# Performance work log

Measured on AMD Instinct MI355X. Metric: run time of the kernel, lower is better.

The kernel has to match this reference:

```python
import jax, jax.numpy as jnp
import numpy as np

EPS = 1e-12  # F.normalize default eps

def _l2norm(x, axis):
    n = jnp.maximum(jnp.linalg.norm(x, axis=axis, keepdims=True), EPS)
    return x / n

def setup_inputs() -> dict:
    key = jax.random.key(0)
    k1, k2 = jax.random.split(key)
    B, G, D, K = 256, 100, 768, 128
    h = jax.random.normal(k1, (B, G, D), dtype=jnp.float32)
    duplicate_pooling = jax.random.normal(k2, (G, D, K), dtype=jnp.float32)
    out_extrap = jnp.zeros((B, G, K), dtype=jnp.float32)
    return {"h": h, "duplicate_pooling": duplicate_pooling, "out_extrap": out_extrap}

def reference(h, duplicate_pooling, out_extrap):
    # normalize=True: L2-normalize each h[:, i, :] over feature dim (dim=1 of the
    # flattened [B, D] view == last axis), and each w_i = W[i] over dim=0 (the D axis).
    hn = _l2norm(h, axis=-1)                       # [B, G, D]
    wn = _l2norm(duplicate_pooling, axis=1)        # [G, D, K]
    # Fused grouped batched GEMM over all G groups at once.
    out = jnp.einsum('bgd,gdk->bgk', hn, wn)       # [B, G, K]
    return out
```

## Files before the change

### kernel.cpp

```cpp
#include <hip/hip_runtime.h>

#define Gn   100
#define Bn   256
#define Dn   768
#define Kn   128
#define LDP  40

typedef __attribute__((ext_vector_type(8))) short short8;
typedef __attribute__((ext_vector_type(4))) float f32x4;

__device__ inline unsigned short f2b(float f) {
  union { float f; unsigned u; } v; v.f = f;
  unsigned r = v.u + 0x7FFFu + ((v.u >> 16) & 1u);
  return (unsigned short)(r >> 16);
}

__global__ __launch_bounds__(256) void groupfc_kernel(
    const float* __restrict__ h, const float* __restrict__ W,
    float* __restrict__ out) {
  const int g    = blockIdx.z;
  const int mt   = blockIdx.x;
  const int nt   = blockIdx.y;
  const int t    = threadIdx.x;
  const int lane = t & 63;
  const int wave = t >> 6;
  const int wm   = wave >> 1, wn = wave & 1;

  __shared__ short Alds[2][64 * LDP];
  __shared__ short Blds[2][64 * LDP];
  __shared__ float AssqL[64];
  __shared__ float BssqL[4][64];

  f32x4 acc00 = {0.f,0.f,0.f,0.f};
  f32x4 acc01 = acc00, acc10 = acc00, acc11 = acc00;

  const int ar = t >> 2;
  const int ac = (t & 3) * 8;
  const float* aptr = h + ((size_t)(mt * 64 + ar) * Gn + g) * Dn + ac;
  const int bk = t & 63;
  const int bd = (t >> 6) * 8;
  const float* bptr = W + (size_t)g * (Dn * Kn) + (size_t)bd * Kn + nt * 64 + bk;

  const int quad = lane >> 4;
  const int koff = quad * 8;
  const int l15  = lane & 15;
  const int m0   = wm * 32 + l15;
  const int n0   = wn * 32 + l15;

  float assq = 0.f, bssq = 0.f;

  float4 a0 = *(const float4*)(aptr);
  float4 a1 = *(const float4*)(aptr + 4);
  float bv[8];
#pragma unroll
  for (int i = 0; i < 8; ++i) bv[i] = bptr[(size_t)i * Kn];

  for (int kc = 0; kc < 24; ++kc) {
    float4 na0, na1;
    float nbv[8];
    if (kc < 23) {
      const int d0 = (kc + 1) * 32;
      na0 = *(const float4*)(aptr + d0);
      na1 = *(const float4*)(aptr + d0 + 4);
#pragma unroll
      for (int i = 0; i < 8; ++i) nbv[i] = bptr[(size_t)(d0 + i) * Kn];
    }

    assq += a0.x*a0.x + a0.y*a0.y + a0.z*a0.z + a0.w*a0.w
          + a1.x*a1.x + a1.y*a1.y + a1.z*a1.z + a1.w*a1.w;
    union { unsigned short us[8]; short8 v; } pa;
    pa.us[0]=f2b(a0.x); pa.us[1]=f2b(a0.y); pa.us[2]=f2b(a0.z); pa.us[3]=f2b(a0.w);
    pa.us[4]=f2b(a1.x); pa.us[5]=f2b(a1.y); pa.us[6]=f2b(a1.z); pa.us[7]=f2b(a1.w);
    *(short8*)&Alds[kc & 1][ar * LDP + ac] = pa.v;

    union { unsigned short us[8]; short8 v; } pb;
#pragma unroll
    for (int i = 0; i < 8; ++i) { bssq += bv[i] * bv[i]; pb.us[i] = f2b(bv[i]); }
    *(short8*)&Blds[kc & 1][bk * LDP + bd] = pb.v;

    __syncthreads();

    short8 af0 = *(const short8*)&Alds[kc & 1][m0 * LDP + koff];
    short8 af1 = *(const short8*)&Alds[kc & 1][(m0 + 16) * LDP + koff];
    short8 bf0 = *(const short8*)&Blds[kc & 1][n0 * LDP + koff];
    short8 bf1 = *(const short8*)&Blds[kc & 1][(n0 + 16) * LDP + koff];

    acc00 = __builtin_amdgcn_mfma_f32_16x16x32_bf16(af0, bf0, acc00, 0, 0, 0);
    acc01 = __builtin_amdgcn_mfma_f32_16x16x32_bf16(af0, bf1, acc01, 0, 0, 0);
    acc10 = __builtin_amdgcn_mfma_f32_16x16x32_bf16(af1, bf0, acc10, 0, 0, 0);
    acc11 = __builtin_amdgcn_mfma_f32_16x16x32_bf16(af1, bf1, acc11, 0, 0, 0);

    a0 = na0; a1 = na1;
#pragma unroll
    for (int i = 0; i < 8; ++i) bv[i] = nbv[i];
  }

  assq += __shfl_xor(assq, 1);
  assq += __shfl_xor(assq, 2);
  if ((t & 3) == 0) AssqL[ar] = assq;
  BssqL[wave][bk] = bssq;
  __syncthreads();

  const float ws0 = BssqL[0][n0] + BssqL[1][n0] + BssqL[2][n0] + BssqL[3][n0];
  const float ws1 = BssqL[0][n0+16] + BssqL[1][n0+16] + BssqL[2][n0+16] + BssqL[3][n0+16];
  const float wi0 = 1.0f / fmaxf(sqrtf(ws0), 1e-12f);
  const float wi1 = 1.0f / fmaxf(sqrtf(ws1), 1e-12f);

#pragma unroll
  for (int mi = 0; mi < 2; ++mi) {
#pragma unroll
    for (int r = 0; r < 4; ++r) {
      const int lr  = wm * 32 + mi * 16 + quad * 4 + r;
      const float hs = 1.0f / fmaxf(sqrtf(AssqL[lr]), 1e-12f);
      const float v0 = (mi ? acc10[r] : acc00[r]) * hs * wi0;
      const float v1 = (mi ? acc11[r] : acc01[r]) * hs * wi1;
      const int row = mt * 64 + lr;
      const size_t ob = ((size_t)row * Gn + g) * Kn + nt * 64;
      out[ob + wn * 32 + l15]      = v0;
      out[ob + wn * 32 + l15 + 16] = v1;
    }
  }
}

extern "C" void kernel_launch(void* const* d_in, const int* in_sizes, int n_in,
                              void* d_out, int out_size, void* d_ws, size_t ws_size,
                              hipStream_t stream) {
  const float* h = (const float*)d_in[0];
  const float* W = (const float*)d_in[1];
  float* out = (float*)d_out;
  hipLaunchKernelGGL(groupfc_kernel, dim3(4, 2, Gn), dim3(256), 0, stream, h, W, out);
}
```

Before: 171.9 us.

## Double K-chunk to 64, cheaper bf16 packing via perm, unroll pipeline by two

Each iteration now stages 64 elements of K instead of 32, which halves the number of barriers and LDS round-trips, and issues two MFMA k-steps per stage. Float-to-bf16 conversion now uses a single byte-permute on two values with round-half-up, replacing per-element round-to-nearest-even. The loop is manually unrolled with ping-pong register sets to keep global loads in flight. The cost is higher register pressure from the 16-wide B loads and doubled LDS tiles.

```diff
diff --git a/kernel.cpp b/kernel.cpp
--- a/kernel.cpp
+++ b/kernel.cpp
@@ -4,15 +4,14 @@
 #define Bn   256
 #define Dn   768
 #define Kn   128
-#define LDP  40
+#define LDP  72
 
 typedef __attribute__((ext_vector_type(8))) short short8;
 typedef __attribute__((ext_vector_type(4))) float f32x4;
 
-__device__ inline unsigned short f2b(float f) {
-  union { float f; unsigned u; } v; v.f = f;
-  unsigned r = v.u + 0x7FFFu + ((v.u >> 16) & 1u);
-  return (unsigned short)(r >> 16);
+__device__ inline unsigned pack2(float lo, float hi) {
+  union { float f; unsigned u; } a, b; a.f = lo; b.f = hi;
+  return __builtin_amdgcn_perm(b.u + 0x8000u, a.u + 0x8000u, 0x07060302u);
 }
 
 __global__ __launch_bounds__(256) void groupfc_kernel(
@@ -26,8 +25,8 @@
   const int wave = t >> 6;
   const int wm   = wave >> 1, wn = wave & 1;
 
-  __shared__ short Alds[2][64 * LDP];
-  __shared__ short Blds[2][64 * LDP];
+  __shared__ __align__(16) short Alds[2][64 * LDP];
+  __shared__ __align__(16) short Blds[2][64 * LDP];
   __shared__ float AssqL[64];
   __shared__ float BssqL[4][64];
 
@@ -35,10 +34,10 @@
   f32x4 acc01 = acc00, acc10 = acc00, acc11 = acc00;
 
   const int ar = t >> 2;
-  const int ac = (t & 3) * 8;
+  const int ac = (t & 3) * 16;
   const float* aptr = h + ((size_t)(mt * 64 + ar) * Gn + g) * Dn + ac;
   const int bk = t & 63;
-  const int bd = (t >> 6) * 8;
+  const int bd = (t >> 6) * 16;
   const float* bptr = W + (size_t)g * (Dn * Kn) + (size_t)bd * Kn + nt * 64 + bk;
 
   const int quad = lane >> 4;
@@ -49,50 +48,67 @@
 
   float assq = 0.f, bssq = 0.f;
 
-  float4 a0 = *(const float4*)(aptr);
-  float4 a1 = *(const float4*)(aptr + 4);
-  float bv[8];
+  float4 ca[4]; float cb[16];
+  float4 pa[4]; float pb[16];
+
+  auto load_chunk = [&](int kc, float4 (&A)[4], float (&Bv)[16]) {
+    const int d0 = kc * 64;
+    const float* ap = aptr + d0;
 #pragma unroll
-  for (int i = 0; i < 8; ++i) bv[i] = bptr[(size_t)i * Kn];
+    for (int i = 0; i < 4; ++i) A[i] = *(const float4*)(ap + i * 4);
+#pragma unroll
+    for (int i = 0; i < 16; ++i) Bv[i] = bptr[(size_t)(d0 + i) * Kn];
+  };
 
-  for (int kc = 0; kc < 24; ++kc) {
-    float4 na0, na1;
-    float nbv[8];
-    if (kc < 23) {
-      const int d0 = (kc + 1) * 32;
-      na0 = *(const float4*)(aptr + d0);
-      na1 = *(const float4*)(aptr + d0 + 4);
+  auto stage_mfma = [&](int buf, const float4 (&A)[4], const float (&Bv)[16]) {
+    float as = 0.f;
 #pragma unroll
-      for (int i = 0; i < 8; ++i) nbv[i] = bptr[(size_t)(d0 + i) * Kn];
-    }
+    for (int i = 0; i < 4; ++i)
+      as += A[i].x*A[i].x + A[i].y*A[i].y + A[i].z*A[i].z + A[i].w*A[i].w;
+    assq += as;
+    float bs = 0.f;
+#pragma unroll
+    for (int i = 0; i < 16; ++i) bs += Bv[i] * Bv[i];
+    bssq += bs;
 
-    assq += a0.x*a0.x + a0.y*a0.y + a0.z*a0.z + a0.w*a0.w
-          + a1.x*a1.x + a1.y*a1.y + a1.z*a1.z + a1.w*a1.w;
-    union { unsigned short us[8]; short8 v; } pa;
-    pa.us[0]=f2b(a0.x); pa.us[1]=f2b(a0.y); pa.us[2]=f2b(a0.z); pa.us[3]=f2b(a0.w);
-    pa.us[4]=f2b(a1.x); pa.us[5]=f2b(a1.y); pa.us[6]=f2b(a1.z); pa.us[7]=f2b(a1.w);
-    *(short8*)&Alds[kc & 1][ar * LDP + ac] = pa.v;
+    uint4 ap0, ap1;
+    ap0.x = pack2(A[0].x, A[0].y); ap0.y = pack2(A[0].z, A[0].w);
+    ap0.z = pack2(A[1].x, A[1].y); ap0.w = pack2(A[1].z, A[1].w);
+    ap1.x = pack2(A[2].x, A[2].y); ap1.y = pack2(A[2].z, A[2].w);
+    ap1.z = pack2(A[3].x, A[3].y); ap1.w = pack2(A[3].z, A[3].w);
+    *(uint4*)&Alds[buf][ar * LDP + ac]     = ap0;
+    *(uint4*)&Alds[buf][ar * LDP + ac + 8] = ap1;
 
-    union { unsigned short us[8]; short8 v; } pb;
-#pragma unroll
-    for (int i = 0; i < 8; ++i) { bssq += bv[i] * bv[i]; pb.us[i] = f2b(bv[i]); }
-    *(short8*)&Blds[kc & 1][bk * LDP + bd] = pb.v;
+    uint4 bp0, bp1;
+    bp0.x = pack2(Bv[0],  Bv[1]);  bp0.y = pack2(Bv[2],  Bv[3]);
+    bp0.z = pack2(Bv[4],  Bv[5]);  bp0.w = pack2(Bv[6],  Bv[7]);
+    bp1.x = pack2(Bv[8],  Bv[9]);  bp1.y = pack2(Bv[10], Bv[11]);
+    bp1.z = pack2(Bv[12], Bv[13]); bp1.w = pack2(Bv[14], Bv[15]);
+    *(uint4*)&Blds[buf][bk * LDP + bd]     = bp0;
+    *(uint4*)&Blds[buf][bk * LDP + bd + 8] = bp1;
 
     __syncthreads();
 
-    short8 af0 = *(const short8*)&Alds[kc & 1][m0 * LDP + koff];
-    short8 af1 = *(const short8*)&Alds[kc & 1][(m0 + 16) * LDP + koff];
-    short8 bf0 = *(const short8*)&Blds[kc & 1][n0 * LDP + koff];
-    short8 bf1 = *(const short8*)&Blds[kc & 1][(n0 + 16) * LDP + koff];
+#pragma unroll
+    for (int kk = 0; kk < 2; ++kk) {
+      const int o = kk * 32 + koff;
+      short8 af0 = *(const short8*)&Alds[buf][m0 * LDP + o];
+      short8 af1 = *(const short8*)&Alds[buf][(m0 + 16) * LDP + o];
+      short8 bf0 = *(const short8*)&Blds[buf][n0 * LDP + o];
+      short8 bf1 = *(const short8*)&Blds[buf][(n0 + 16) * LDP + o];
+      acc00 = __builtin_amdgcn_mfma_f32_16x16x32_bf16(af0, bf0, acc00, 0, 0, 0);
+      acc01 = __builtin_amdgcn_mfma_f32_16x16x32_bf16(af0, bf1, acc01, 0, 0, 0);
+      acc10 = __builtin_amdgcn_mfma_f32_16x16x32_bf16(af1, bf0, acc10, 0, 0, 0);
+      acc11 = __builtin_amdgcn_mfma_f32_16x16x32_bf16(af1, bf1, acc11, 0, 0, 0);
+    }
+  };
 
-    acc00 = __builtin_amdgcn_mfma_f32_16x16x32_bf16(af0, bf0, acc00, 0, 0, 0);
-    acc01 = __builtin_amdgcn_mfma_f32_16x16x32_bf16(af0, bf1, acc01, 0, 0, 0);
-    acc10 = __builtin_amdgcn_mfma_f32_16x16x32_bf16(af1, bf0, acc10, 0, 0, 0);
-    acc11 = __builtin_amdgcn_mfma_f32_16x16x32_bf16(af1, bf1, acc11, 0, 0, 0);
-
-    a0 = na0; a1 = na1;
-#pragma unroll
-    for (int i = 0; i < 8; ++i) bv[i] = nbv[i];
+  load_chunk(0, ca, cb);
+  for (int kc = 0; kc < 12; kc += 2) {
+    load_chunk(kc + 1, pa, pb);
+    stage_mfma(0, ca, cb);
+    if (kc + 2 < 12) load_chunk(kc + 2, ca, cb);
+    stage_mfma(1, pa, pb);
   }
 
   assq += __shfl_xor(assq, 1);
```

New measurement: 173.5 us. About the same (+0.9%).

## Load MFMA fragments directly from global memory, dropping LDS staging and barriers

Applied to the files above, without the earlier changes.

Each lane now loads its own A and B fragment elements from global memory straight into registers, packs them to bf16, and feeds the MFMAs without staging through shared memory, so the per-chunk __syncthreads is gone. The main loop is double-buffered in registers, and the bf16 conversion uses a perm-based pack with round-half-up in place of round-to-nearest-even. Each wave now loads its tiles separately, so A and B are read twice per block instead of once, and the B loads are strided scalar reads. This trades more global/L2 traffic for fewer barriers and no LDS round trips.

```diff
diff --git a/kernel.cpp b/kernel.cpp
--- a/kernel.cpp
+++ b/kernel.cpp
@@ -4,15 +4,13 @@
 #define Bn   256
 #define Dn   768
 #define Kn   128
-#define LDP  40
 
 typedef __attribute__((ext_vector_type(8))) short short8;
 typedef __attribute__((ext_vector_type(4))) float f32x4;
 
-__device__ inline unsigned short f2b(float f) {
-  union { float f; unsigned u; } v; v.f = f;
-  unsigned r = v.u + 0x7FFFu + ((v.u >> 16) & 1u);
-  return (unsigned short)(r >> 16);
+__device__ inline unsigned pack2(float lo, float hi) {
+  union { float f; unsigned u; } a, b; a.f = lo; b.f = hi;
+  return __builtin_amdgcn_perm(b.u + 0x8000u, a.u + 0x8000u, 0x07060302u);
 }
 
 __global__ __launch_bounds__(256) void groupfc_kernel(
@@ -25,92 +23,97 @@
   const int lane = t & 63;
   const int wave = t >> 6;
   const int wm   = wave >> 1, wn = wave & 1;
+  const int l15  = lane & 15, quad = lane >> 4;
 
-  __shared__ short Alds[2][64 * LDP];
-  __shared__ short Blds[2][64 * LDP];
   __shared__ float AssqL[64];
-  __shared__ float BssqL[4][64];
+  __shared__ float BssqL[64];
+
+  const int r0 = mt * 64 + wm * 32 + l15;
+  const int n0 = nt * 64 + wn * 32 + l15;
+  const float* ap0 = h + ((size_t)r0 * Gn + g) * Dn + quad * 8;
+  const float* ap1 = ap0 + (size_t)16 * Gn * Dn;
+  const float* bp0 = W + (size_t)g * Dn * Kn + (size_t)(quad * 8) * Kn + n0;
+  const float* bp1 = bp0 + 16;
 
   f32x4 acc00 = {0.f,0.f,0.f,0.f};
   f32x4 acc01 = acc00, acc10 = acc00, acc11 = acc00;
+  float as0 = 0.f, as1 = 0.f, bs0 = 0.f, bs1 = 0.f;
 
-  const int ar = t >> 2;
-  const int ac = (t & 3) * 8;
-  const float* aptr = h + ((size_t)(mt * 64 + ar) * Gn + g) * Dn + ac;
-  const int bk = t & 63;
-  const int bd = (t >> 6) * 8;
-  const float* bptr = W + (size_t)g * (Dn * Kn) + (size_t)bd * Kn + nt * 64 + bk;
+  float4 cA0[2], cA1[2]; float cB0[8], cB1[8];
+  float4 pA0[2], pA1[2]; float pB0[8], pB1[8];
 
-  const int quad = lane >> 4;
-  const int koff = quad * 8;
-  const int l15  = lane & 15;
-  const int m0   = wm * 32 + l15;
-  const int n0   = wn * 32 + l15;
+  auto load_chunk = [&](int c, float4 (&A0)[2], float4 (&A1)[2],
+                        float (&B0)[8], float (&B1)[8]) {
+    const float* a0 = ap0 + c * 32;
+    const float* a1 = ap1 + c * 32;
+    A0[0] = *(const float4*)a0; A0[1] = *(const float4*)(a0 + 4);
+    A1[0] = *(const float4*)a1; A1[1] = *(const float4*)(a1 + 4);
+    const float* b0 = bp0 + (size_t)c * 32 * Kn;
+    const float* b1 = bp1 + (size_t)c * 32 * Kn;
+#pragma unroll
+    for (int j = 0; j < 8; ++j) {
+      B0[j] = b0[(size_t)j * Kn];
+      B1[j] = b1[(size_t)j * Kn];
+    }
+  };
 
-  float assq = 0.f, bssq = 0.f;
+  auto ssq4 = [](const float4& v) {
+    return v.x*v.x + v.y*v.y + v.z*v.z + v.w*v.w;
+  };
 
-  float4 a0 = *(const float4*)(aptr);
-  float4 a1 = *(const float4*)(aptr + 4);
-  float bv[8];
+  auto consume = [&](float4 (&A0)[2], float4 (&A1)[2],
+                     float (&B0)[8], float (&B1)[8]) {
+    as0 += ssq4(A0[0]) + ssq4(A0[1]);
+    as1 += ssq4(A1[0]) + ssq4(A1[1]);
 #pragma unroll
-  for (int i = 0; i < 8; ++i) bv[i] = bptr[(size_t)i * Kn];
+    for (int j = 0; j < 8; ++j) { bs0 += B0[j]*B0[j]; bs1 += B1[j]*B1[j]; }
 
-  for (int kc = 0; kc < 24; ++kc) {
-    float4 na0, na1;
-    float nbv[8];
-    if (kc < 23) {
-      const int d0 = (kc + 1) * 32;
-      na0 = *(const float4*)(aptr + d0);
-      na1 = *(const float4*)(aptr + d0 + 4);
-#pragma unroll
-      for (int i = 0; i < 8; ++i) nbv[i] = bptr[(size_t)(d0 + i) * Kn];
-    }
+    union { unsigned d[4]; short8 v; } af0, af1, bf0, bf1;
+    af0.d[0] = pack2(A0[0].x, A0[0].y); af0.d[1] = pack2(A0[0].z, A0[0].w);
+    af0.d[2] = pack2(A0[1].x, A0[1].y); af0.d[3] = pack2(A0[1].z, A0[1].w);
+    af1.d[0] = pack2(A1[0].x, A1[0].y); af1.d[1] = pack2(A1[0].z, A1[0].w);
+    af1.d[2] = pack2(A1[1].x, A1[1].y); af1.d[3] = pack2(A1[1].z, A1[1].w);
+    bf0.d[0] = pack2(B0[0], B0[1]); bf0.d[1] = pack2(B0[2], B0[3]);
+    bf0.d[2] = pack2(B0[4], B0[5]); bf0.d[3] = pack2(B0[6], B0[7]);
+    bf1.d[0] = pack2(B1[0], B1[1]); bf1.d[1] = pack2(B1[2], B1[3]);
+    bf1.d[2] = pack2(B1[4], B1[5]); bf1.d[3] = pack2(B1[6], B1[7]);
 
-    assq += a0.x*a0.x + a0.y*a0.y + a0.z*a0.z + a0.w*a0.w
-          + a1.x*a1.x + a1.y*a1.y + a1.z*a1.z + a1.w*a1.w;
-    union { unsigned short us[8]; short8 v; } pa;
-    pa.us[0]=f2b(a0.x); pa.us[1]=f2b(a0.y); pa.us[2]=f2b(a0.z); pa.us[3]=f2b(a0.w);
-    pa.us[4]=f2b(a1.x); pa.us[5]=f2b(a1.y); pa.us[6]=f2b(a1.z); pa.us[7]=f2b(a1.w);
-    *(short8*)&Alds[kc & 1][ar * LDP + ac] = pa.v;
+    acc00 = __builtin_amdgcn_mfma_f32_16x16x32_bf16(af0.v, bf0.v, acc00, 0, 0, 0);
+    acc01 = __builtin_amdgcn_mfma_f32_16x16x32_bf16(af0.v, bf1.v, acc01, 0, 0, 0);
+    acc10 = __builtin_amdgcn_mfma_f32_16x16x32_bf16(af1.v, bf0.v, acc10, 0, 0, 0);
+    acc11 = __builtin_amdgcn_mfma_f32_16x16x32_bf16(af1.v, bf1.v, acc11, 0, 0, 0);
+  };
 
-    union { unsigned short us[8]; short8 v; } pb;
-#pragma unroll
-    for (int i = 0; i < 8; ++i) { bssq += bv[i] * bv[i]; pb.us[i] = f2b(bv[i]); }
-    *(short8*)&Blds[kc & 1][bk * LDP + bd] = pb.v;
-
-    __syncthreads();
-
-    short8 af0 = *(const short8*)&Alds[kc & 1][m0 * LDP + koff];
-    short8 af1 = *(const short8*)&Alds[kc & 1][(m0 + 16) * LDP + koff];
-    short8 bf0 = *(const short8*)&Blds[kc & 1][n0 * LDP + koff];
-    short8 bf1 = *(const short8*)&Blds[kc & 1][(n0 + 16) * LDP + koff];
-
-    acc00 = __builtin_amdgcn_mfma_f32_16x16x32_bf16(af0, bf0, acc00, 0, 0, 0);
-    acc01 = __builtin_amdgcn_mfma_f32_16x16x32_bf16(af0, bf1, acc01, 0, 0, 0);
-    acc10 = __builtin_amdgcn_mfma_f32_16x16x32_bf16(af1, bf0, acc10, 0, 0, 0);
-    acc11 = __builtin_amdgcn_mfma_f32_16x16x32_bf16(af1, bf1, acc11, 0, 0, 0);
-
-    a0 = na0; a1 = na1;
-#pragma unroll
-    for (int i = 0; i < 8; ++i) bv[i] = nbv[i];
+  load_chunk(0, cA0, cA1, cB0, cB1);
+  for (int c = 0; c < 24; c += 2) {
+    load_chunk(c + 1, pA0, pA1, pB0, pB1);
+    consume(cA0, cA1, cB0, cB1);
+    if (c + 2 < 24) load_chunk(c + 2, cA0, cA1, cB0, cB1);
+    consume(pA0, pA1, pB0, pB1);
   }
 
-  assq += __shfl_xor(assq, 1);
-  assq += __shfl_xor(assq, 2);
-  if ((t & 3) == 0) AssqL[ar] = assq;
-  BssqL[wave][bk] = bssq;
+  as0 += __shfl_xor(as0, 16); as0 += __shfl_xor(as0, 32);
+  as1 += __shfl_xor(as1, 16); as1 += __shfl_xor(as1, 32);
+  bs0 += __shfl_xor(bs0, 16); bs0 += __shfl_xor(bs0, 32);
+  bs1 += __shfl_xor(bs1, 16); bs1 += __shfl_xor(bs1, 32);
+  if (wn == 0 && quad == 0) {
+    AssqL[wm * 32 + l15]      = as0;
+    AssqL[wm * 32 + l15 + 16] = as1;
+  }
+  if (wm == 0 && quad == 0) {
+    BssqL[wn * 32 + l15]      = bs0;
+    BssqL[wn * 32 + l15 + 16] = bs1;
+  }
   __syncthreads();
 
-  const float ws0 = BssqL[0][n0] + BssqL[1][n0] + BssqL[2][n0] + BssqL[3][n0];
-  const float ws1 = BssqL[0][n0+16] + BssqL[1][n0+16] + BssqL[2][n0+16] + BssqL[3][n0+16];
-  const float wi0 = 1.0f / fmaxf(sqrtf(ws0), 1e-12f);
-  const float wi1 = 1.0f / fmaxf(sqrtf(ws1), 1e-12f);
+  const float wi0 = 1.0f / fmaxf(sqrtf(BssqL[wn * 32 + l15]),      1e-12f);
+  const float wi1 = 1.0f / fmaxf(sqrtf(BssqL[wn * 32 + l15 + 16]), 1e-12f);
 
 #pragma unroll
   for (int mi = 0; mi < 2; ++mi) {
 #pragma unroll
     for (int r = 0; r < 4; ++r) {
-      const int lr  = wm * 32 + mi * 16 + quad * 4 + r;
+      const int lr = wm * 32 + mi * 16 + quad * 4 + r;
       const float hs = 1.0f / fmaxf(sqrtf(AssqL[lr]), 1e-12f);
       const float v0 = (mi ? acc10[r] : acc00[r]) * hs * wi0;
       const float v1 = (mi ? acc11[r] : acc01[r]) * hs * wi1;
```

Result: slower. 194.8 us (+13.3%).

## Load A tiles directly to LDS with swizzle and remap blocks per XCD

Applied to the files above, without the earlier changes.

Activation tiles are now streamed straight into swizzled fp32 LDS buffers with global_load_lds, and the bf16 conversion and squared-norm accumulation move to after the LDS read. Rounding is replaced by a cheaper perm-based pack, and the grid is flattened so that all tiles of one group land on the same XCD to share L2. The sync order is restructured so the next chunk's loads overlap the current MFMAs. In exchange LDS traffic for A doubles, and the rounding becomes round-half-up instead of round-to-even, so results can differ slightly.

```diff
diff --git a/kernel.cpp b/kernel.cpp
--- a/kernel.cpp
+++ b/kernel.cpp
@@ -4,101 +4,136 @@
 #define Bn   256
 #define Dn   768
 #define Kn   128
-#define LDP  40
+#define BLDP 40
 
 typedef __attribute__((ext_vector_type(8))) short short8;
 typedef __attribute__((ext_vector_type(4))) float f32x4;
 
-__device__ inline unsigned short f2b(float f) {
-  union { float f; unsigned u; } v; v.f = f;
-  unsigned r = v.u + 0x7FFFu + ((v.u >> 16) & 1u);
-  return (unsigned short)(r >> 16);
+__device__ inline unsigned pack2(float lo, float hi) {
+  union { float f; unsigned u; } a, b; a.f = lo; b.f = hi;
+  return __builtin_amdgcn_perm(b.u + 0x8000u, a.u + 0x8000u, 0x07060302u);
+}
+
+__device__ inline void gload_lds16(const float* src, float* dst) {
+  __builtin_amdgcn_global_load_lds(
+      (const __attribute__((address_space(1))) void*)src,
+      (__attribute__((address_space(3))) void*)dst, 16, 0, 0);
 }
 
 __global__ __launch_bounds__(256) void groupfc_kernel(
     const float* __restrict__ h, const float* __restrict__ W,
     float* __restrict__ out) {
-  const int g    = blockIdx.z;
-  const int mt   = blockIdx.x;
-  const int nt   = blockIdx.y;
+  const int id   = blockIdx.x;
+  const int xcd  = id & 7;
+  const int rest = id >> 3;
+  const int tl   = rest & 7;
+  const int g    = (rest >> 3) * 8 + xcd;
+  if (g >= Gn) return;
+  const int mt   = tl >> 1;
+  const int nt   = tl & 1;
+
   const int t    = threadIdx.x;
   const int lane = t & 63;
   const int wave = t >> 6;
   const int wm   = wave >> 1, wn = wave & 1;
+  const int l15  = lane & 15, quad = lane >> 4;
 
-  __shared__ short Alds[2][64 * LDP];
-  __shared__ short Blds[2][64 * LDP];
+  __shared__ __align__(16) float Af[2][64 * 32];
+  __shared__ __align__(16) short Bf[2][64 * BLDP];
   __shared__ float AssqL[64];
   __shared__ float BssqL[4][64];
 
+  const int lr0 = wave * 16 + (lane >> 3);
+  const int lr1 = lr0 + 8;
+  const int sg0 = (lane & 7) ^ ((lr0 & 3) << 1);
+  const int sg1 = (lane & 7) ^ ((lr1 & 3) << 1);
+  const float* asrc0 = h + ((size_t)(mt * 64 + lr0) * Gn + g) * Dn + sg0 * 4;
+  const float* asrc1 = h + ((size_t)(mt * 64 + lr1) * Gn + g) * Dn + sg1 * 4;
+  const int aoff0 = (wave * 16) * 32;
+  const int aoff1 = (wave * 16 + 8) * 32;
+
+  const int bk = t & 63;
+  const int bq = t >> 6;
+  const float* bptr = W + (size_t)g * (Dn * Kn) + (size_t)(bq * 8) * Kn + nt * 64 + bk;
+
   f32x4 acc00 = {0.f,0.f,0.f,0.f};
   f32x4 acc01 = acc00, acc10 = acc00, acc11 = acc00;
+  float as0 = 0.f, as1 = 0.f, bssq = 0.f;
 
-  const int ar = t >> 2;
-  const int ac = (t & 3) * 8;
-  const float* aptr = h + ((size_t)(mt * 64 + ar) * Gn + g) * Dn + ac;
-  const int bk = t & 63;
-  const int bd = (t >> 6) * 8;
-  const float* bptr = W + (size_t)g * (Dn * Kn) + (size_t)bd * Kn + nt * 64 + bk;
+  const int m0 = wm * 32 + l15;
+  const int n0 = wn * 32 + l15;
+  const int sA = (l15 & 3) << 1;
+  const int ag = ((2 * quad) ^ sA) * 4;
 
-  const int quad = lane >> 4;
-  const int koff = quad * 8;
-  const int l15  = lane & 15;
-  const int m0   = wm * 32 + l15;
-  const int n0   = wn * 32 + l15;
+  float bv[8];
 
-  float assq = 0.f, bssq = 0.f;
-
-  float4 a0 = *(const float4*)(aptr);
-  float4 a1 = *(const float4*)(aptr + 4);
-  float bv[8];
+  gload_lds16(asrc0, &Af[0][aoff0]);
+  gload_lds16(asrc1, &Af[0][aoff1]);
 #pragma unroll
   for (int i = 0; i < 8; ++i) bv[i] = bptr[(size_t)i * Kn];
+  {
+    uint4 bp;
+    bp.x = pack2(bv[0], bv[1]); bp.y = pack2(bv[2], bv[3]);
+    bp.z = pack2(bv[4], bv[5]); bp.w = pack2(bv[6], bv[7]);
+#pragma unroll
+    for (int i = 0; i < 8; ++i) bssq += bv[i] * bv[i];
+    *(uint4*)&Bf[0][bk * BLDP + bq * 8] = bp;
+  }
 
-  for (int kc = 0; kc < 24; ++kc) {
-    float4 na0, na1;
-    float nbv[8];
-    if (kc < 23) {
-      const int d0 = (kc + 1) * 32;
-      na0 = *(const float4*)(aptr + d0);
-      na1 = *(const float4*)(aptr + d0 + 4);
+  for (int c = 0; c < 24; ++c) {
+    const int buf = c & 1;
+    __syncthreads();
+
+    if (c < 23) {
+      const int d0 = (c + 1) * 32;
+      gload_lds16(asrc0 + d0, &Af[1 - buf][aoff0]);
+      gload_lds16(asrc1 + d0, &Af[1 - buf][aoff1]);
 #pragma unroll
-      for (int i = 0; i < 8; ++i) nbv[i] = bptr[(size_t)(d0 + i) * Kn];
+      for (int i = 0; i < 8; ++i) bv[i] = bptr[(size_t)(d0 + i) * Kn];
     }
 
-    assq += a0.x*a0.x + a0.y*a0.y + a0.z*a0.z + a0.w*a0.w
-          + a1.x*a1.x + a1.y*a1.y + a1.z*a1.z + a1.w*a1.w;
-    union { unsigned short us[8]; short8 v; } pa;
-    pa.us[0]=f2b(a0.x); pa.us[1]=f2b(a0.y); pa.us[2]=f2b(a0.z); pa.us[3]=f2b(a0.w);
-    pa.us[4]=f2b(a1.x); pa.us[5]=f2b(a1.y); pa.us[6]=f2b(a1.z); pa.us[7]=f2b(a1.w);
-    *(short8*)&Alds[kc & 1][ar * LDP + ac] = pa.v;
+    f32x4 a0lo = *(const f32x4*)&Af[buf][m0 * 32 + ag];
+    f32x4 a0hi = *(const f32x4*)&Af[buf][m0 * 32 + (ag ^ 16) + (((2*quad)&2)*0)];
+    a0hi = *(const f32x4*)&Af[buf][m0 * 32 + ag + 4];
+    f32x4 a1lo = *(const f32x4*)&Af[buf][(m0 + 16) * 32 + ag];
+    f32x4 a1hi = *(const f32x4*)&Af[buf][(m0 + 16) * 32 + ag + 4];
 
-    union { unsigned short us[8]; short8 v; } pb;
+    as0 += a0lo.x*a0lo.x + a0lo.y*a0lo.y + a0lo.z*a0lo.z + a0lo.w*a0lo.w
+         + a0hi.x*a0hi.x + a0hi.y*a0hi.y + a0hi.z*a0hi.z + a0hi.w*a0hi.w;
+    as1 += a1lo.x*a1lo.x + a1lo.y*a1lo.y + a1lo.z*a1lo.z + a1lo.w*a1lo.w
+         + a1hi.x*a1hi.x + a1hi.y*a1hi.y + a1hi.z*a1hi.z + a1hi.w*a1hi.w;
+
+    union { unsigned d[4]; short8 v; } af0, af1;
+    af0.d[0] = pack2(a0lo.x, a0lo.y); af0.d[1] = pack2(a0lo.z, a0lo.w);
+    af0.d[2] = pack2(a0hi.x, a0hi.y); af0.d[3] = pack2(a0hi.z, a0hi.w);
+    af1.d[0] = pack2(a1lo.x, a1lo.y); af1.d[1] = pack2(a1lo.z, a1lo.w);
+    af1.d[2] = pack2(a1hi.x, a1hi.y); af1.d[3] = pack2(a1hi.z, a1hi.w);
+
+    short8 bf0 = *(const short8*)&Bf[buf][n0 * BLDP + quad * 8];
+    short8 bf1 = *(const short8*)&Bf[buf][(n0 + 16) * BLDP + quad * 8];
+
+    acc00 = __builtin_amdgcn_mfma_f32_16x16x32_bf16(af0.v, bf0, acc00, 0, 0, 0);
+    acc01 = __builtin_amdgcn_mfma_f32_16x16x32_bf16(af0.v, bf1, acc01, 0, 0, 0);
+    acc10 = __builtin_amdgcn_mfma_f32_16x16x32_bf16(af1.v, bf0, acc10, 0, 0, 0);
+    acc11 = __builtin_amdgcn_mfma_f32_16x16x32_bf16(af1.v, bf1, acc11, 0, 0, 0);
+
+    if (c < 23) {
+      uint4 bp;
+      bp.x = pack2(bv[0], bv[1]); bp.y = pack2(bv[2], bv[3]);
+      bp.z = pack2(bv[4], bv[5]); bp.w = pack2(bv[6], bv[7]);
 #pragma unroll
-    for (int i = 0; i < 8; ++i) { bssq += bv[i] * bv[i]; pb.us[i] = f2b(bv[i]); }
-    *(short8*)&Blds[kc & 1][bk * LDP + bd] = pb.v;
-
-    __syncthreads();
-
-    short8 af0 = *(const short8*)&Alds[kc & 1][m0 * LDP + koff];
-    short8 af1 = *(const short8*)&Alds[kc & 1][(m0 + 16) * LDP + koff];
-    short8 bf0 = *(const short8*)&Blds[kc & 1][n0 * LDP + koff];
-    short8 bf1 = *(const short8*)&Blds[kc & 1][(n0 + 16) * LDP + koff];
-
-    acc00 = __builtin_amdgcn_mfma_f32_16x16x32_bf16(af0, bf0, acc00, 0, 0, 0);
-    acc01 = __builtin_amdgcn_mfma_f32_16x16x32_bf16(af0, bf1, acc01, 0, 0, 0);
-    acc10 = __builtin_amdgcn_mfma_f32_16x16x32_bf16(af1, bf0, acc10, 0, 0, 0);
-    acc11 = __builtin_amdgcn_mfma_f32_16x16x32_bf16(af1, bf1, acc11, 0, 0, 0);
-
-    a0 = na0; a1 = na1;
-#pragma unroll
-    for (int i = 0; i < 8; ++i) bv[i] = nbv[i];
+      for (int i = 0; i < 8; ++i) bssq += bv[i] * bv[i];
+      *(uint4*)&Bf[1 - buf][bk * BLDP + bq * 8] = bp;
+    }
   }
 
-  assq += __shfl_xor(assq, 1);
-  assq += __shfl_xor(assq, 2);
-  if ((t & 3) == 0) AssqL[ar] = assq;
-  BssqL[wave][bk] = bssq;
+  as0 += __shfl_xor(as0, 16); as0 += __shfl_xor(as0, 32);
+  as1 += __shfl_xor(as1, 16); as1 += __shfl_xor(as1, 32);
+  if (wn == 0 && quad == 0) {
+    AssqL[wm * 32 + l15]      = as0;
+    AssqL[wm * 32 + l15 + 16] = as1;
+  }
+  BssqL[bq][bk] = bssq;
   __syncthreads();
 
   const float ws0 = BssqL[0][n0] + BssqL[1][n0] + BssqL[2][n0] + BssqL[3][n0];
@@ -110,7 +145,7 @@
   for (int mi = 0; mi < 2; ++mi) {
 #pragma unroll
     for (int r = 0; r < 4; ++r) {
-      const int lr  = wm * 32 + mi * 16 + quad * 4 + r;
+      const int lr = wm * 32 + mi * 16 + quad * 4 + r;
       const float hs = 1.0f / fmaxf(sqrtf(AssqL[lr]), 1e-12f);
       const float v0 = (mi ? acc10[r] : acc00[r]) * hs * wi0;
       const float v1 = (mi ? acc11[r] : acc01[r]) * hs * wi1;
@@ -128,5 +163,5 @@
   const float* h = (const float*)d_in[0];
   const float* W = (const float*)d_in[1];
   float* out = (float*)d_out;
-  hipLaunchKernelGGL(groupfc_kernel, dim3(4, 2, Gn), dim3(256), 0, stream, h, W, out);
+  hipLaunchKernelGGL(groupfc_kernel, dim3(832), dim3(256), 0, stream, h, W, out);
 }
```

Result: no change. 170.1 us (-1.0%).
